# Optimization experiments

Hardware: AMD Instinct MI355X
Metric: run time of the kernel (lower is better)

## Reference

```python
import jax, jax.numpy as jnp
import numpy as np

N = 50000      # nodes
E = 600000     # edges (avg degree 12)
IN, H, OUT = 128, 256, 256


def setup_inputs() -> dict:
    key = jax.random.key(0)
    ks = jax.random.split(key, 9)
    glorot = lambda k, shp: jax.random.uniform(
        k, shp, jnp.float32, -1.0, 1.0) * np.sqrt(6.0 / (shp[0] + shp[1]))
    return {
        "x": jax.random.normal(ks[0], (N, IN), jnp.float32),
        "src": jax.random.randint(ks[1], (E,), 0, N, jnp.int32),
        "dst": jax.random.randint(ks[2], (E,), 0, N, jnp.int32),
        "W_conv": glorot(ks[3], (IN, H)),
        "b_conv": jnp.zeros((H,), jnp.float32),
        "W_fc": glorot(ks[4], (H, H)),
        "b_fc": jax.random.uniform(ks[5], (H,), jnp.float32, -1, 1) / np.sqrt(H),
        "W_fc2": glorot(ks[6], (H, OUT)),
        "b_fc2": jax.random.uniform(ks[7], (OUT,), jnp.float32, -1, 1) / np.sqrt(OUT),
    }


def reference(x, src, dst, W_conv, b_conv, W_fc, b_fc, W_fc2, b_fc2):
    ones = jnp.ones((E,), x.dtype)
    # dgl GraphConv, norm='both': D_in^{-1/2} A D_out^{-1/2} X W + b
    deg_out = jax.ops.segment_sum(ones, src, num_segments=N)
    deg_in = jax.ops.segment_sum(ones, dst, num_segments=N)
    norm_src = jax.lax.rsqrt(jnp.maximum(deg_out, 1.0))  # [N]
    norm_dst = jax.lax.rsqrt(jnp.maximum(deg_in, 1.0))   # [N]
    feat = x * norm_src[:, None]                          # [N, IN]
    agg = jax.ops.segment_sum(feat[src], dst, num_segments=N)  # gather+scatter SpMM
    h = agg * norm_dst[:, None]
    h = h @ W_conv + b_conv                               # GraphConv weight+bias
    # num_nonl_layers == 2 branch
    h = jax.nn.relu(h) @ W_fc + b_fc
    h = jax.nn.relu(h) @ W_fc2 + b_fc2
    return h
```

## Files before the change

### kernel.cpp

```cpp
#include <hip/hip_runtime.h>

#define NN 50000
#define NE 600000
#define FIN 128
#define CAPS 128
#define CAPU 64
#define PW1 136
#define PW2 264
#define PRE_BLOCKS 3125
#define WP_BLOCKS  640

typedef __attribute__((ext_vector_type(8))) short bf16x8;
typedef __attribute__((ext_vector_type(4))) float f32x4;

__device__ __forceinline__ unsigned short f2bf(float f) {
    union { float f; unsigned int i; } v; v.f = f;
    return (unsigned short)((v.i + 0x7FFFu + ((v.i >> 16) & 1u)) >> 16);
}
__device__ __forceinline__ float bflo(unsigned int u) {
    union { unsigned int i; float f; } v; v.i = u << 16; return v.f;
}
__device__ __forceinline__ float bfhi(unsigned int u) {
    union { unsigned int i; float f; } v; v.i = u & 0xffff0000u; return v.f;
}


__global__ __launch_bounds__(256)
void bin_kernel(const int* __restrict__ src, const int* __restrict__ dst,
                int* __restrict__ cnt_in, int* __restrict__ cnt_out,
                int* __restrict__ csr_src) {
    int e = blockIdx.x * 256 + threadIdx.x;
    if (e < NE) {
        int s = src[e], d = dst[e];
        int p = atomicAdd(&cnt_in[d], 1);
        if (p < CAPU) csr_src[d * CAPS + p] = s;
        atomicAdd(&cnt_out[s], 1);
    }
}

__global__ __launch_bounds__(256)
void prep_kernel(const float* __restrict__ x, const int* __restrict__ cnt_out,
                 unsigned short* __restrict__ xn,
                 const float* __restrict__ Wc, const float* __restrict__ W1,
                 const float* __restrict__ W2, unsigned short* __restrict__ wout) {
    int b = blockIdx.x;
    if (b < PRE_BLOCKS) {
        int idx = b * 256 + threadIdx.x;
        int row = idx >> 4;
        float sc = rsqrtf(fmaxf((float)cnt_out[row], 1.0f));
        const float4* xp = (const float4*)(x + (size_t)idx * 8);
        float4 a = xp[0], c = xp[1];
        unsigned int w0 = f2bf(a.x * sc) | ((unsigned int)f2bf(a.y * sc) << 16);
        unsigned int w1 = f2bf(a.z * sc) | ((unsigned int)f2bf(a.w * sc) << 16);
        unsigned int w2 = f2bf(c.x * sc) | ((unsigned int)f2bf(c.y * sc) << 16);
        unsigned int w3 = f2bf(c.z * sc) | ((unsigned int)f2bf(c.w * sc) << 16);
        uint4 o = {w0, w1, w2, w3};
        *(uint4*)(xn + (size_t)idx * 8) = o;
    } else {
        int t = (b - PRE_BLOCKS) * 256 + threadIdx.x;
        if (t < 32768) {
            int n = t >> 7, k = t & 127;
            wout[t] = f2bf(Wc[k * 256 + n]);
        } else if (t < 98304) {
            int i = t - 32768; int n = i >> 8, k = i & 255;
            wout[32768 + i] = f2bf(W1[k * 256 + n]);
        } else if (t < 163840) {
            int i = t - 98304; int n = i >> 8, k = i & 255;
            wout[98304 + i] = f2bf(W2[k * 256 + n]);
        }
    }
}

__global__ __launch_bounds__(256)
void gather_kernel(const unsigned short* __restrict__ xn,
                   const int* __restrict__ csr_src,
                   const int* __restrict__ cnt_in,
                   char* __restrict__ slotbase) {
    int tid  = threadIdx.x;
    int grp  = tid >> 5;
    int lane = tid & 31;
    int r = blockIdx.x * 8 + grp;
    if (r >= NN) return;
    int deg = cnt_in[r];
    float nd = rsqrtf(fmaxf((float)deg, 1.0f));
    int cnt = deg > CAPU ? CAPU : deg;
    const int* bucket = csr_src + (size_t)r * CAPS;
    const unsigned short* xb = xn + lane * 4;
    float4 acc = {0.f, 0.f, 0.f, 0.f};
    for (int j0 = 0; j0 < cnt; j0 += 32) {
        int c = cnt - j0; if (c > 32) c = 32;
        int sv = (lane < c) ? bucket[j0 + lane] : 0;
        int i = 0;
        for (; i + 4 <= c; i += 4) {
            int s0 = __shfl(sv, i,     32), s1 = __shfl(sv, i + 1, 32);
            int s2 = __shfl(sv, i + 2, 32), s3 = __shfl(sv, i + 3, 32);
            uint2 w0 = *(const uint2*)(xb + (size_t)s0 * FIN);
            uint2 w1 = *(const uint2*)(xb + (size_t)s1 * FIN);
            uint2 w2 = *(const uint2*)(xb + (size_t)s2 * FIN);
            uint2 w3 = *(const uint2*)(xb + (size_t)s3 * FIN);
            acc.x += bflo(w0.x); acc.y += bfhi(w0.x); acc.z += bflo(w0.y); acc.w += bfhi(w0.y);
            acc.x += bflo(w1.x); acc.y += bfhi(w1.x); acc.z += bflo(w1.y); acc.w += bfhi(w1.y);
            acc.x += bflo(w2.x); acc.y += bfhi(w2.x); acc.z += bflo(w2.y); acc.w += bfhi(w2.y);
            acc.x += bflo(w3.x); acc.y += bfhi(w3.x); acc.z += bflo(w3.y); acc.w += bfhi(w3.y);
        }
        for (; i < c; ++i) {
            int s = __shfl(sv, i, 32);
            uint2 w = *(const uint2*)(xb + (size_t)s * FIN);
            acc.x += bflo(w.x); acc.y += bfhi(w.x);
            acc.z += bflo(w.y); acc.w += bfhi(w.y);
        }
    }
    unsigned short o[4];
    o[0] = f2bf(acc.x * nd); o[1] = f2bf(acc.y * nd);
    o[2] = f2bf(acc.z * nd); o[3] = f2bf(acc.w * nd);
    *(uint2*)(slotbase + (size_t)r * 1024 + 768 + lane * 8) = *(const uint2*)o;
}

__global__ __launch_bounds__(256)
void gather_fb_kernel(const float* __restrict__ x, const int* __restrict__ csr_src,
                      const int* __restrict__ cnt_in, const int* __restrict__ cnt_out,
                      char* __restrict__ slotbase) {
    int tid  = threadIdx.x;
    int grp  = tid >> 5;
    int lane = tid & 31;
    int r = blockIdx.x * 8 + grp;
    if (r >= NN) return;
    int deg = cnt_in[r];
    float nd = rsqrtf(fmaxf((float)deg, 1.0f));
    int cnt = deg > CAPU ? CAPU : deg;
    const int* bucket = csr_src + (size_t)r * CAPS;
    const float* xb = x + lane * 4;
    float4 acc = {0.f, 0.f, 0.f, 0.f};
    for (int j0 = 0; j0 < cnt; j0 += 32) {
        int c = cnt - j0; if (c > 32) c = 32;
        int sv = 0; float nsl = 0.f;
        if (lane < c) {
            sv  = bucket[j0 + lane];
            nsl = rsqrtf(fmaxf((float)cnt_out[sv], 1.0f));
        }
        for (int i = 0; i < c; ++i) {
            int   s  = __shfl(sv,  i, 32);
            float ns = __shfl(nsl, i, 32);
            float4 xv = *(const float4*)(xb + (size_t)s * FIN);
            acc.x += xv.x * ns; acc.y += xv.y * ns;
            acc.z += xv.z * ns; acc.w += xv.w * ns;
        }
    }
    unsigned short o[4];
    o[0] = f2bf(acc.x * nd); o[1] = f2bf(acc.y * nd);
    o[2] = f2bf(acc.z * nd); o[3] = f2bf(acc.w * nd);
    *(uint2*)(slotbase + (size_t)r * 1024 + 768 + lane * 8) = *(const uint2*)o;
}

__global__ __launch_bounds__(256)
void wprep_kernel(const float* __restrict__ Wc, const float* __restrict__ W1,
                  const float* __restrict__ W2, unsigned short* __restrict__ o) {
    int t = blockIdx.x * 256 + threadIdx.x;
    if (t < 32768) {
        int n = t >> 7, k = t & 127;
        o[t] = f2bf(Wc[k * 256 + n]);
    } else if (t < 98304) {
        int i = t - 32768; int n = i >> 8, k = i & 255;
        o[32768 + i] = f2bf(W1[k * 256 + n]);
    } else if (t < 163840) {
        int i = t - 98304; int n = i >> 8, k = i & 255;
        o[98304 + i] = f2bf(W2[k * 256 + n]);
    }
}

__global__ __launch_bounds__(256)
void gemm1_kernel(char* slotbase, const unsigned short* __restrict__ Wct,
                  const float* __restrict__ bc) {
    __shared__ short wsh[64 * PW1];
    int tid = threadIdx.x;
    int wave = tid >> 6, lane = tid & 63;
    int quad = lane >> 4, l16 = lane & 15;
    int m0 = blockIdx.x * 128 + wave * 32;
    bf16x8 a[2][4];
    #pragma unroll
    for (int g = 0; g < 2; ++g) {
        int arow = m0 + g * 16 + l16; if (arow >= NN) arow = NN - 1;
        const unsigned short* Ap =
            (const unsigned short*)(slotbase + (size_t)arow * 1024 + 768) + quad * 8;
        #pragma unroll
        for (int i = 0; i < 4; ++i) a[g][i] = *(const bf16x8*)(Ap + i * 32);
    }
    int sc = tid >> 2, sq = tid & 3;
    #pragma unroll 1
    for (int p = 0; p < 2; ++p) {
        int n0 = blockIdx.y * 128 + p * 64;
        __syncthreads();
        {
            const unsigned short* g = Wct + (size_t)(n0 + sc) * 128 + sq * 32;
            #pragma unroll
            for (int j = 0; j < 4; ++j)
                *(bf16x8*)&wsh[sc * PW1 + sq * 32 + j * 8] = *(const bf16x8*)(g + j * 8);
        }
        __syncthreads();
        f32x4 acc[2][4] = {};
        #pragma unroll
        for (int i = 0; i < 4; ++i) {
            int k0 = i * 32;
            bf16x8 b0 = *(const bf16x8*)&wsh[( 0 + l16) * PW1 + quad * 8 + k0];
            bf16x8 b1 = *(const bf16x8*)&wsh[(16 + l16) * PW1 + quad * 8 + k0];
            bf16x8 b2 = *(const bf16x8*)&wsh[(32 + l16) * PW1 + quad * 8 + k0];
            bf16x8 b3 = *(const bf16x8*)&wsh[(48 + l16) * PW1 + quad * 8 + k0];
            #pragma unroll
            for (int g = 0; g < 2; ++g) {
                acc[g][0] = __builtin_amdgcn_mfma_f32_16x16x32_bf16(a[g][i], b0, acc[g][0], 0, 0, 0);
                acc[g][1] = __builtin_amdgcn_mfma_f32_16x16x32_bf16(a[g][i], b1, acc[g][1], 0, 0, 0);
                acc[g][2] = __builtin_amdgcn_mfma_f32_16x16x32_bf16(a[g][i], b2, acc[g][2], 0, 0, 0);
                acc[g][3] = __builtin_amdgcn_mfma_f32_16x16x32_bf16(a[g][i], b3, acc[g][3], 0, 0, 0);
            }
        }
        #pragma unroll
        for (int c = 0; c < 4; ++c) {
            int col = n0 + c * 16 + l16;
            float bv = bc[col];
            #pragma unroll
            for (int g = 0; g < 2; ++g) {
                #pragma unroll
                for (int r2 = 0; r2 < 4; ++r2) {
                    int rr = m0 + g * 16 + quad * 4 + r2;
                    if (rr < NN)
                        *(unsigned short*)(slotbase + (size_t)rr * 1024 + 2 * col) =
                            f2bf(fmaxf(acc[g][c][r2] + bv, 0.0f));
                }
            }
        }
    }
}

__global__ __launch_bounds__(256)
void gemm2_kernel(char* slotbase, const unsigned short* __restrict__ Wt,
                  const float* __restrict__ bias) {
    __shared__ short wsh[64 * PW2];
    int tid = threadIdx.x;
    int wave = tid >> 6, lane = tid & 63;
    int quad = lane >> 4, l16 = lane & 15;
    int m0 = blockIdx.x * 128 + wave * 32;
    bf16x8 a[2][8];
    #pragma unroll
    for (int g = 0; g < 2; ++g) {
        int arow = m0 + g * 16 + l16; if (arow >= NN) arow = NN - 1;
        const unsigned short* Ap =
            (const unsigned short*)(slotbase + (size_t)arow * 1024) + quad * 8;
        #pragma unroll
        for (int i = 0; i < 8; ++i) a[g][i] = *(const bf16x8*)(Ap + i * 32);
    }
    int sc = tid >> 2, sq = tid & 3;
    #pragma unroll 1
    for (int p = 0; p < 2; ++p) {
        int n0 = blockIdx.y * 128 + p * 64;
        __syncthreads();
        {
            const unsigned short* g = Wt + (size_t)(n0 + sc) * 256 + sq * 64;
            #pragma unroll
            for (int j = 0; j < 8; ++j)
                *(bf16x8*)&wsh[sc * PW2 + sq * 64 + j * 8] = *(const bf16x8*)(g + j * 8);
        }
        __syncthreads();
        f32x4 acc[2][4] = {};
        #pragma unroll
        for (int i = 0; i < 8; ++i) {
            int k0 = i * 32;
            bf16x8 b0 = *(const bf16x8*)&wsh[( 0 + l16) * PW2 + quad * 8 + k0];
            bf16x8 b1 = *(const bf16x8*)&wsh[(16 + l16) * PW2 + quad * 8 + k0];
            bf16x8 b2 = *(const bf16x8*)&wsh[(32 + l16) * PW2 + quad * 8 + k0];
            bf16x8 b3 = *(const bf16x8*)&wsh[(48 + l16) * PW2 + quad * 8 + k0];
            #pragma unroll
            for (int g = 0; g < 2; ++g) {
                acc[g][0] = __builtin_amdgcn_mfma_f32_16x16x32_bf16(a[g][i], b0, acc[g][0], 0, 0, 0);
                acc[g][1] = __builtin_amdgcn_mfma_f32_16x16x32_bf16(a[g][i], b1, acc[g][1], 0, 0, 0);
                acc[g][2] = __builtin_amdgcn_mfma_f32_16x16x32_bf16(a[g][i], b2, acc[g][2], 0, 0, 0);
                acc[g][3] = __builtin_amdgcn_mfma_f32_16x16x32_bf16(a[g][i], b3, acc[g][3], 0, 0, 0);
            }
        }
        #pragma unroll
        for (int c = 0; c < 4; ++c) {
            int col = n0 + c * 16 + l16;
            float bv = bias[col];
            #pragma unroll
            for (int g = 0; g < 2; ++g) {
                #pragma unroll
                for (int r2 = 0; r2 < 4; ++r2) {
                    int rr = m0 + g * 16 + quad * 4 + r2;
                    if (rr < NN)
                        *(unsigned short*)(slotbase + (size_t)rr * 1024 + 512 + 2 * col) =
                            f2bf(fmaxf(acc[g][c][r2] + bv, 0.0f));
                }
            }
        }
    }
}

__global__ __launch_bounds__(256)
void gemm3_kernel(char* slotbase, const unsigned short* __restrict__ Wt,
                  const float* __restrict__ bias) {
    __shared__ short wsh[64 * PW2];
    int tid = threadIdx.x;
    int wave = tid >> 6, lane = tid & 63;
    int quad = lane >> 4, l16 = lane & 15;
    int m0 = blockIdx.x * 64 + wave * 16;
    int arow = m0 + l16; if (arow >= NN) arow = NN - 1;
    const unsigned short* Ap =
        (const unsigned short*)(slotbase + (size_t)arow * 1024 + 512) + quad * 8;
    bf16x8 a[8];
    #pragma unroll
    for (int i = 0; i < 8; ++i) a[i] = *(const bf16x8*)(Ap + i * 32);
    int sc = tid >> 2, sq = tid & 3;
    #pragma unroll 1
    for (int p = 0; p < 4; ++p) {
        __syncthreads();
        {
            const unsigned short* g = Wt + (size_t)(p * 64 + sc) * 256 + sq * 64;
            #pragma unroll
            for (int j = 0; j < 8; ++j)
                *(bf16x8*)&wsh[sc * PW2 + sq * 64 + j * 8] = *(const bf16x8*)(g + j * 8);
        }
        __syncthreads();
        f32x4 ac0 = {0.f,0.f,0.f,0.f}, ac1 = ac0, ac2 = ac0, ac3 = ac0;
        #pragma unroll
        for (int i = 0; i < 8; ++i) {
            int k0 = i * 32;
            bf16x8 b0 = *(const bf16x8*)&wsh[( 0 + l16) * PW2 + quad * 8 + k0];
            bf16x8 b1 = *(const bf16x8*)&wsh[(16 + l16) * PW2 + quad * 8 + k0];
            bf16x8 b2 = *(const bf16x8*)&wsh[(32 + l16) * PW2 + quad * 8 + k0];
            bf16x8 b3 = *(const bf16x8*)&wsh[(48 + l16) * PW2 + quad * 8 + k0];
            ac0 = __builtin_amdgcn_mfma_f32_16x16x32_bf16(a[i], b0, ac0, 0, 0, 0);
            ac1 = __builtin_amdgcn_mfma_f32_16x16x32_bf16(a[i], b1, ac1, 0, 0, 0);
            ac2 = __builtin_amdgcn_mfma_f32_16x16x32_bf16(a[i], b2, ac2, 0, 0, 0);
            ac3 = __builtin_amdgcn_mfma_f32_16x16x32_bf16(a[i], b3, ac3, 0, 0, 0);
        }
        int n0 = p * 64;
        f32x4 accs[4] = {ac0, ac1, ac2, ac3};
        #pragma unroll
        for (int c = 0; c < 4; ++c) {
            int col = n0 + c * 16 + l16;
            float bv = bias[col];
            #pragma unroll
            for (int r2 = 0; r2 < 4; ++r2) {
                int rr = m0 + quad * 4 + r2;
                if (rr < NN)
                    *(float*)(slotbase + (size_t)rr * 1024 + 4 * col) = accs[c][r2] + bv;
            }
        }
    }
}


extern "C" void kernel_launch(void* const* d_in, const int* in_sizes, int n_in,
                              void* d_out, int out_size, void* d_ws, size_t ws_size,
                              hipStream_t stream) {
    const float* x      = (const float*)d_in[0];
    const int*   src    = (const int*)d_in[1];
    const int*   dst    = (const int*)d_in[2];
    const float* W_conv = (const float*)d_in[3];
    const float* b_conv = (const float*)d_in[4];
    const float* W_fc   = (const float*)d_in[5];
    const float* b_fc   = (const float*)d_in[6];
    const float* W_fc2  = (const float*)d_in[7];
    const float* b_fc2  = (const float*)d_in[8];
    char* slotbase = (char*)d_out;

    int* csr_src = (int*)(slotbase + 16000000);

    char* ws = (char*)d_ws;
    int* cnt_out = (int*)(ws + 0);
    int* cnt_in  = (int*)(ws + 204800);

    hipMemsetAsync(d_ws, 0, 409600, stream);

    bin_kernel<<<(NE + 255) / 256, 256, 0, stream>>>(src, dst, cnt_in, cnt_out,
                                                     csr_src);

    dim3 g12((NN + 127) / 128, 2);
    if (ws_size >= 13537408) {
        unsigned short* xn  = (unsigned short*)(ws + 409728);
        unsigned short* Wct = (unsigned short*)(ws + 13209728);
        unsigned short* W1t = Wct + 32768;
        unsigned short* W2t = Wct + 98304;
        prep_kernel<<<PRE_BLOCKS + WP_BLOCKS, 256, 0, stream>>>(
            x, cnt_out, xn, W_conv, W_fc, W_fc2, Wct);
        gather_kernel<<<(NN + 7) / 8, 256, 0, stream>>>(xn, csr_src, cnt_in,
                                                        slotbase);
        gemm1_kernel<<<g12, 256, 0, stream>>>(slotbase, Wct, b_conv);
        gemm2_kernel<<<g12, 256, 0, stream>>>(slotbase, W1t, b_fc);
        gemm3_kernel<<<(NN + 63) / 64, 256, 0, stream>>>(slotbase, W2t, b_fc2);
    } else {
        unsigned short* Wct = (unsigned short*)(ws + 0);
        unsigned short* W1t = Wct + 32768;
        unsigned short* W2t = Wct + 98304;
        gather_fb_kernel<<<(NN + 7) / 8, 256, 0, stream>>>(x, csr_src, cnt_in,
                                                           cnt_out, slotbase);
        wprep_kernel<<<WP_BLOCKS, 256, 0, stream>>>(W_conv, W_fc, W_fc2, Wct);
        gemm1_kernel<<<g12, 256, 0, stream>>>(slotbase, Wct, b_conv);
        gemm2_kernel<<<g12, 256, 0, stream>>>(slotbase, W1t, b_fc);
        gemm3_kernel<<<(NN + 63) / 64, 256, 0, stream>>>(slotbase, W2t, b_fc2);
    }
}
```

Before: 257.0 us.

## Fuse three MLP GEMMs into one kernel keeping intermediates in LDS

Replaces the three separate GEMM kernels with one fused kernel per 64-row tile. The hidden activations after each layer stay in shared memory (hsh) instead of being written to and re-read from global memory, and two kernel launches are removed. In exchange, each block uses more LDS, which may lower occupancy, and each wave now handles a single 16-row group, so it no longer reuses each weight fragment across two row groups.

Result: faster. 243.8 us (-5.1%).

```diff
diff --git a/kernel.cpp b/kernel.cpp
--- a/kernel.cpp
+++ b/kernel.cpp
@@ -7,6 +7,7 @@
 #define CAPU 64
 #define PW1 136
 #define PW2 264
+#define PH  264
 #define PRE_BLOCKS 3125
 #define WP_BLOCKS  640
 
@@ -169,178 +170,144 @@
 }
 
 __global__ __launch_bounds__(256)
-void gemm1_kernel(char* slotbase, const unsigned short* __restrict__ Wct,
-                  const float* __restrict__ bc) {
-    __shared__ short wsh[64 * PW1];
+void fused_mlp_kernel(char* slotbase,
+                      const unsigned short* __restrict__ Wct,
+                      const unsigned short* __restrict__ W1t,
+                      const unsigned short* __restrict__ W2t,
+                      const float* __restrict__ bc,
+                      const float* __restrict__ b1,
+                      const float* __restrict__ b2) {
+    __shared__ short wsh[64 * PW2];
+    __shared__ short hsh[64 * PH];
     int tid = threadIdx.x;
     int wave = tid >> 6, lane = tid & 63;
     int quad = lane >> 4, l16 = lane & 15;
-    int m0 = blockIdx.x * 128 + wave * 32;
-    bf16x8 a[2][4];
-    #pragma unroll
-    for (int g = 0; g < 2; ++g) {
-        int arow = m0 + g * 16 + l16; if (arow >= NN) arow = NN - 1;
+    int B0 = blockIdx.x * 64;
+    int m0 = wave * 16;
+    int sc = tid >> 2, sq = tid & 3;
+
+    int arow = B0 + m0 + l16; if (arow >= NN) arow = NN - 1;
+    bf16x8 a1[4];
+    {
         const unsigned short* Ap =
             (const unsigned short*)(slotbase + (size_t)arow * 1024 + 768) + quad * 8;
         #pragma unroll
-        for (int i = 0; i < 4; ++i) a[g][i] = *(const bf16x8*)(Ap + i * 32);
-    }
-    int sc = tid >> 2, sq = tid & 3;
+        for (int i = 0; i < 4; ++i) a1[i] = *(const bf16x8*)(Ap + i * 32);
+    }
+
     #pragma unroll 1
-    for (int p = 0; p < 2; ++p) {
-        int n0 = blockIdx.y * 128 + p * 64;
+    for (int p = 0; p < 4; ++p) {
         __syncthreads();
         {
-            const unsigned short* g = Wct + (size_t)(n0 + sc) * 128 + sq * 32;
+            const unsigned short* g = Wct + (size_t)(p * 64 + sc) * 128 + sq * 32;
             #pragma unroll
             for (int j = 0; j < 4; ++j)
                 *(bf16x8*)&wsh[sc * PW1 + sq * 32 + j * 8] = *(const bf16x8*)(g + j * 8);
         }
         __syncthreads();
-        f32x4 acc[2][4] = {};
+        f32x4 ac0 = {0.f,0.f,0.f,0.f}, ac1 = ac0, ac2 = ac0, ac3 = ac0;
         #pragma unroll
         for (int i = 0; i < 4; ++i) {
             int k0 = i * 32;
             bf16x8 b0 = *(const bf16x8*)&wsh[( 0 + l16) * PW1 + quad * 8 + k0];
-            bf16x8 b1 = *(const bf16x8*)&wsh[(16 + l16) * PW1 + quad * 8 + k0];
-            bf16x8 b2 = *(const bf16x8*)&wsh[(32 + l16) * PW1 + quad * 8 + k0];
-            bf16x8 b3 = *(const bf16x8*)&wsh[(48 + l16) * PW1 + quad * 8 + k0];
-            #pragma unroll
-            for (int g = 0; g < 2; ++g) {
-                acc[g][0] = __builtin_amdgcn_mfma_f32_16x16x32_bf16(a[g][i], b0, acc[g][0], 0, 0, 0);
-                acc[g][1] = __builtin_amdgcn_mfma_f32_16x16x32_bf16(a[g][i], b1, acc[g][1], 0, 0, 0);
-                acc[g][2] = __builtin_amdgcn_mfma_f32_16x16x32_bf16(a[g][i], b2, acc[g][2], 0, 0, 0);
-                acc[g][3] = __builtin_amdgcn_mfma_f32_16x16x32_bf16(a[g][i], b3, acc[g][3], 0, 0, 0);
-            }
-        }
+            bf16x8 b1v = *(const bf16x8*)&wsh[(16 + l16) * PW1 + quad * 8 + k0];
+            bf16x8 b2v = *(const bf16x8*)&wsh[(32 + l16) * PW1 + quad * 8 + k0];
+            bf16x8 b3v = *(const bf16x8*)&wsh[(48 + l16) * PW1 + quad * 8 + k0];
+            ac0 = __builtin_amdgcn_mfma_f32_16x16x32_bf16(a1[i], b0,  ac0, 0, 0, 0);
+            ac1 = __builtin_amdgcn_mfma_f32_16x16x32_bf16(a1[i], b1v, ac1, 0, 0, 0);
+            ac2 = __builtin_amdgcn_mfma_f32_16x16x32_bf16(a1[i], b2v, ac2, 0, 0, 0);
+            ac3 = __builtin_amdgcn_mfma_f32_16x16x32_bf16(a1[i], b3v, ac3, 0, 0, 0);
+        }
+        f32x4 accs[4] = {ac0, ac1, ac2, ac3};
         #pragma unroll
         for (int c = 0; c < 4; ++c) {
-            int col = n0 + c * 16 + l16;
+            int col = p * 64 + c * 16 + l16;
             float bv = bc[col];
             #pragma unroll
-            for (int g = 0; g < 2; ++g) {
-                #pragma unroll
-                for (int r2 = 0; r2 < 4; ++r2) {
-                    int rr = m0 + g * 16 + quad * 4 + r2;
-                    if (rr < NN)
-                        *(unsigned short*)(slotbase + (size_t)rr * 1024 + 2 * col) =
-                            f2bf(fmaxf(acc[g][c][r2] + bv, 0.0f));
-                }
-            }
-        }
-    }
-}
-
-__global__ __launch_bounds__(256)
-void gemm2_kernel(char* slotbase, const unsigned short* __restrict__ Wt,
-                  const float* __restrict__ bias) {
-    __shared__ short wsh[64 * PW2];
-    int tid = threadIdx.x;
-    int wave = tid >> 6, lane = tid & 63;
-    int quad = lane >> 4, l16 = lane & 15;
-    int m0 = blockIdx.x * 128 + wave * 32;
-    bf16x8 a[2][8];
-    #pragma unroll
-    for (int g = 0; g < 2; ++g) {
-        int arow = m0 + g * 16 + l16; if (arow >= NN) arow = NN - 1;
-        const unsigned short* Ap =
-            (const unsigned short*)(slotbase + (size_t)arow * 1024) + quad * 8;
-        #pragma unroll
-        for (int i = 0; i < 8; ++i) a[g][i] = *(const bf16x8*)(Ap + i * 32);
-    }
-    int sc = tid >> 2, sq = tid & 3;
+            for (int r2 = 0; r2 < 4; ++r2)
+                hsh[(m0 + quad * 4 + r2) * PH + col] =
+                    (short)f2bf(fmaxf(accs[c][r2] + bv, 0.0f));
+        }
+    }
+
+    bf16x8 a2[8];
     #pragma unroll 1
-    for (int p = 0; p < 2; ++p) {
-        int n0 = blockIdx.y * 128 + p * 64;
+    for (int p = 0; p < 4; ++p) {
         __syncthreads();
         {
-            const unsigned short* g = Wt + (size_t)(n0 + sc) * 256 + sq * 64;
+            const unsigned short* g = W1t + (size_t)(p * 64 + sc) * 256 + sq * 64;
             #pragma unroll
             for (int j = 0; j < 8; ++j)
                 *(bf16x8*)&wsh[sc * PW2 + sq * 64 + j * 8] = *(const bf16x8*)(g + j * 8);
         }
         __syncthreads();
-        f32x4 acc[2][4] = {};
+        if (p == 0) {
+            #pragma unroll
+            for (int i = 0; i < 8; ++i)
+                a2[i] = *(const bf16x8*)&hsh[(m0 + l16) * PH + quad * 8 + i * 32];
+        }
+        f32x4 ac0 = {0.f,0.f,0.f,0.f}, ac1 = ac0, ac2 = ac0, ac3 = ac0;
         #pragma unroll
         for (int i = 0; i < 8; ++i) {
             int k0 = i * 32;
             bf16x8 b0 = *(const bf16x8*)&wsh[( 0 + l16) * PW2 + quad * 8 + k0];
-            bf16x8 b1 = *(const bf16x8*)&wsh[(16 + l16) * PW2 + quad * 8 + k0];
-            bf16x8 b2 = *(const bf16x8*)&wsh[(32 + l16) * PW2 + quad * 8 + k0];
-            bf16x8 b3 = *(const bf16x8*)&wsh[(48 + l16) * PW2 + quad * 8 + k0];
-            #pragma unroll
-            for (int g = 0; g < 2; ++g) {
-                acc[g][0] = __builtin_amdgcn_mfma_f32_16x16x32_bf16(a[g][i], b0, acc[g][0], 0, 0, 0);
-                acc[g][1] = __builtin_amdgcn_mfma_f32_16x16x32_bf16(a[g][i], b1, acc[g][1], 0, 0, 0);
-                acc[g][2] = __builtin_amdgcn_mfma_f32_16x16x32_bf16(a[g][i], b2, acc[g][2], 0, 0, 0);
-                acc[g][3] = __builtin_amdgcn_mfma_f32_16x16x32_bf16(a[g][i], b3, acc[g][3], 0, 0, 0);
-            }
-        }
+            bf16x8 b1v = *(const bf16x8*)&wsh[(16 + l16) * PW2 + quad * 8 + k0];
+            bf16x8 b2v = *(const bf16x8*)&wsh[(32 + l16) * PW2 + quad * 8 + k0];
+            bf16x8 b3v = *(const bf16x8*)&wsh[(48 + l16) * PW2 + quad * 8 + k0];
+            ac0 = __builtin_amdgcn_mfma_f32_16x16x32_bf16(a2[i], b0,  ac0, 0, 0, 0);
+            ac1 = __builtin_amdgcn_mfma_f32_16x16x32_bf16(a2[i], b1v, ac1, 0, 0, 0);
+            ac2 = __builtin_amdgcn_mfma_f32_16x16x32_bf16(a2[i], b2v, ac2, 0, 0, 0);
+            ac3 = __builtin_amdgcn_mfma_f32_16x16x32_bf16(a2[i], b3v, ac3, 0, 0, 0);
+        }
+        f32x4 accs[4] = {ac0, ac1, ac2, ac3};
         #pragma unroll
         for (int c = 0; c < 4; ++c) {
-            int col = n0 + c * 16 + l16;
-            float bv = bias[col];
-            #pragma unroll
-            for (int g = 0; g < 2; ++g) {
-                #pragma unroll
-                for (int r2 = 0; r2 < 4; ++r2) {
-                    int rr = m0 + g * 16 + quad * 4 + r2;
-                    if (rr < NN)
-                        *(unsigned short*)(slotbase + (size_t)rr * 1024 + 512 + 2 * col) =
-                            f2bf(fmaxf(acc[g][c][r2] + bv, 0.0f));
-                }
-            }
-        }
-    }
-}
-
-__global__ __launch_bounds__(256)
-void gemm3_kernel(char* slotbase, const unsigned short* __restrict__ Wt,
-                  const float* __restrict__ bias) {
-    __shared__ short wsh[64 * PW2];
-    int tid = threadIdx.x;
-    int wave = tid >> 6, lane = tid & 63;
-    int quad = lane >> 4, l16 = lane & 15;
-    int m0 = blockIdx.x * 64 + wave * 16;
-    int arow = m0 + l16; if (arow >= NN) arow = NN - 1;
-    const unsigned short* Ap =
-        (const unsigned short*)(slotbase + (size_t)arow * 1024 + 512) + quad * 8;
-    bf16x8 a[8];
-    #pragma unroll
-    for (int i = 0; i < 8; ++i) a[i] = *(const bf16x8*)(Ap + i * 32);
-    int sc = tid >> 2, sq = tid & 3;
+            int col = p * 64 + c * 16 + l16;
+            float bv = b1[col];
+            #pragma unroll
+            for (int r2 = 0; r2 < 4; ++r2)
+                hsh[(m0 + quad * 4 + r2) * PH + col] =
+                    (short)f2bf(fmaxf(accs[c][r2] + bv, 0.0f));
+        }
+    }
+
+    bf16x8 a3[8];
     #pragma unroll 1
     for (int p = 0; p < 4; ++p) {
         __syncthreads();
         {
-            const unsigned short* g = Wt + (size_t)(p * 64 + sc) * 256 + sq * 64;
+            const unsigned short* g = W2t + (size_t)(p * 64 + sc) * 256 + sq * 64;
             #pragma unroll
             for (int j = 0; j < 8; ++j)
                 *(bf16x8*)&wsh[sc * PW2 + sq * 64 + j * 8] = *(const bf16x8*)(g + j * 8);
         }
         __syncthreads();
+        if (p == 0) {
+            #pragma unroll
+            for (int i = 0; i < 8; ++i)
+                a3[i] = *(const bf16x8*)&hsh[(m0 + l16) * PH + quad * 8 + i * 32];
+        }
         f32x4 ac0 = {0.f,0.f,0.f,0.f}, ac1 = ac0, ac2 = ac0, ac3 = ac0;
         #pragma unroll
         for (int i = 0; i < 8; ++i) {
             int k0 = i * 32;
             bf16x8 b0 = *(const bf16x8*)&wsh[( 0 + l16) * PW2 + quad * 8 + k0];
-            bf16x8 b1 = *(const bf16x8*)&wsh[(16 + l16) * PW2 + quad * 8 + k0];
-            bf16x8 b2 = *(const bf16x8*)&wsh[(32 + l16) * PW2 + quad * 8 + k0];
-            bf16x8 b3 = *(const bf16x8*)&wsh[(48 + l16) * PW2 + quad * 8 + k0];
-            ac0 = __builtin_amdgcn_mfma_f32_16x16x32_bf16(a[i], b0, ac0, 0, 0, 0);
-            ac1 = __builtin_amdgcn_mfma_f32_16x16x32_bf16(a[i], b1, ac1, 0, 0, 0);
-            ac2 = __builtin_amdgcn_mfma_f32_16x16x32_bf16(a[i], b2, ac2, 0, 0, 0);
-            ac3 = __builtin_amdgcn_mfma_f32_16x16x32_bf16(a[i], b3, ac3, 0, 0, 0);
-        }
-        int n0 = p * 64;
+            bf16x8 b1v = *(const bf16x8*)&wsh[(16 + l16) * PW2 + quad * 8 + k0];
+            bf16x8 b2v = *(const bf16x8*)&wsh[(32 + l16) * PW2 + quad * 8 + k0];
+            bf16x8 b3v = *(const bf16x8*)&wsh[(48 + l16) * PW2 + quad * 8 + k0];
+            ac0 = __builtin_amdgcn_mfma_f32_16x16x32_bf16(a3[i], b0,  ac0, 0, 0, 0);
+            ac1 = __builtin_amdgcn_mfma_f32_16x16x32_bf16(a3[i], b1v, ac1, 0, 0, 0);
+            ac2 = __builtin_amdgcn_mfma_f32_16x16x32_bf16(a3[i], b2v, ac2, 0, 0, 0);
+            ac3 = __builtin_amdgcn_mfma_f32_16x16x32_bf16(a3[i], b3v, ac3, 0, 0, 0);
+        }
         f32x4 accs[4] = {ac0, ac1, ac2, ac3};
         #pragma unroll
         for (int c = 0; c < 4; ++c) {
-            int col = n0 + c * 16 + l16;
-            float bv = bias[col];
+            int col = p * 64 + c * 16 + l16;
+            float bv = b2[col];
             #pragma unroll
             for (int r2 = 0; r2 < 4; ++r2) {
-                int rr = m0 + quad * 4 + r2;
+                int rr = B0 + m0 + quad * 4 + r2;
                 if (rr < NN)
                     *(float*)(slotbase + (size_t)rr * 1024 + 4 * col) = accs[c][r2] + bv;
             }
@@ -374,7 +341,7 @@
     bin_kernel<<<(NE + 255) / 256, 256, 0, stream>>>(src, dst, cnt_in, cnt_out,
                                                      csr_src);
 
-    dim3 g12((NN + 127) / 128, 2);
+    int nb = (NN + 63) / 64;
     if (ws_size >= 13537408) {
         unsigned short* xn  = (unsigned short*)(ws + 409728);
         unsigned short* Wct = (unsigned short*)(ws + 13209728);
@@ -384,9 +351,8 @@
             x, cnt_out, xn, W_conv, W_fc, W_fc2, Wct);
         gather_kernel<<<(NN + 7) / 8, 256, 0, stream>>>(xn, csr_src, cnt_in,
                                                         slotbase);
-        gemm1_kernel<<<g12, 256, 0, stream>>>(slotbase, Wct, b_conv);
-        gemm2_kernel<<<g12, 256, 0, stream>>>(slotbase, W1t, b_fc);
-        gemm3_kernel<<<(NN + 63) / 64, 256, 0, stream>>>(slotbase, W2t, b_fc2);
+        fused_mlp_kernel<<<nb, 256, 0, stream>>>(slotbase, Wct, W1t, W2t,
+                                                 b_conv, b_fc, b_fc2);
     } else {
         unsigned short* Wct = (unsigned short*)(ws + 0);
         unsigned short* W1t = Wct + 32768;
@@ -394,8 +360,7 @@
         gather_fb_kernel<<<(NN + 7) / 8, 256, 0, stream>>>(x, csr_src, cnt_in,
                                                            cnt_out, slotbase);
         wprep_kernel<<<WP_BLOCKS, 256, 0, stream>>>(W_conv, W_fc, W_fc2, Wct);
-        gemm1_kernel<<<g12, 256, 0, stream>>>(slotbase, Wct, b_conv);
-        gemm2_kernel<<<g12, 256, 0, stream>>>(slotbase, W1t, b_fc);
-        gemm3_kernel<<<(NN + 63) / 64, 256, 0, stream>>>(slotbase, W2t, b_fc2);
-    }
-}
+        fused_mlp_kernel<<<nb, 256, 0, stream>>>(slotbase, Wct, W1t, W2t,
+                                                 b_conv, b_fc, b_fc2);
+    }
+}
```
